# Kernel optimization log

Measured on AMD Instinct MI355X. Metric: run time of the kernel, lower is better.

## Reference

```python
import jax, jax.numpy as jnp
import numpy as np

N, E, K = 1048576, 64, 8        # tokens, experts, top-k
TEMP = 1.0                       # default temperature_scheduler returns 1.0
NEG = -1e16                      # masked-logit fill from the original code
EPS = 1e-8


def setup_inputs() -> dict:
    key = jax.random.key(0)
    k1, k2 = jax.random.split(key)
    inputs = jax.random.normal(k1, (N, E), dtype=jnp.float32)
    # Gumbel noise exactly as sample_gumbel(): -log(-log(U + 1e-8) + 1e-8)
    u = jax.random.uniform(k2, (N, E), dtype=jnp.float32)
    noise = -jnp.log(-jnp.log(u + EPS) + EPS)
    return {"inputs": inputs, "noise": noise}


def reference(inputs, noise):
    # Gumbel-perturbed softmax over experts (training path)
    probs = jax.nn.softmax((inputs + noise) / TEMP, axis=1)          # [N, E]
    # top-k expert selection on perturbed probs (indices only matter)
    _, top_k_idx = jax.lax.top_k(probs, K)                           # [N, K]
    # one-hot-sum mask built via scatter instead of materializing [N, K, E]
    rows = jnp.arange(inputs.shape[0])[:, None]                      # [N, 1]
    mask = jnp.zeros_like(inputs).at[rows, top_k_idx].set(1.0)       # [N, E]
    # keep ORIGINAL (un-noised) logits at selected experts, -1e16 elsewhere
    sparse_inputs = jnp.where(mask > 0.0, inputs, NEG)
    # renormalize over the selected experts
    return jax.nn.softmax(sparse_inputs, axis=1)
```

## Files before the change

### kernel.cpp

```cpp
#include <hip/hip_runtime.h>
#include <cstdint>

typedef float float4v __attribute__((ext_vector_type(4)));

__device__ __forceinline__ uint32_t mono32(float x) {
    int32_t b = __float_as_int(x);
    return (uint32_t)(b ^ ((b >> 31) | 0x80000000));
}

__global__ __launch_bounds__(256, 4)
void gumbel_topk_softmax_kernel(const float* __restrict__ gin,
                                const float* __restrict__ gnz,
                                float* __restrict__ gout) {
    const int t   = threadIdx.x;
    const int c   = t & 3;
    const size_t row = (size_t)blockIdx.x * 64 + (t >> 2);
    const size_t base = row * 64 + (size_t)c * 16;

    const float4v* a4 = (const float4v*)(gin + base);
    const float4v* b4 = (const float4v*)(gnz + base);

    float4v vin[4], vnz[4];
#pragma unroll
    for (int q = 0; q < 4; ++q) vin[q] = a4[q];
#pragma unroll
    for (int q = 0; q < 4; ++q) vnz[q] = b4[q];

    float keys[16];
    float heap[8];
#pragma unroll
    for (int u = 0; u < 8; ++u) heap[u] = -INFINITY;
#pragma unroll
    for (int q = 0; q < 4; ++q)
#pragma unroll
        for (int i = 0; i < 4; ++i) {
            float s = vin[q][i] + vnz[q][i];
            keys[q * 4 + i] = s;
#pragma unroll
            for (int u = 0; u < 8; ++u) {
                float h = heap[u];
                heap[u] = fmaxf(h, s);
                s       = fminf(h, s);
            }
        }

#define CEX(A, B) { float mx = fmaxf(heap[A], heap[B]);                       \
                    float mn = fminf(heap[A], heap[B]);                       \
                    heap[A] = mx; heap[B] = mn; }
#pragma unroll
    for (int m = 1; m <= 2; m <<= 1) {
        float part[8];
#pragma unroll
        for (int u = 0; u < 8; ++u) part[u] = __shfl_xor(heap[7 - u], m);
#pragma unroll
        for (int u = 0; u < 8; ++u) heap[u] = fmaxf(heap[u], part[u]);
        CEX(0, 4) CEX(1, 5) CEX(2, 6) CEX(3, 7)
        CEX(0, 2) CEX(1, 3) CEX(4, 6) CEX(5, 7)
        CEX(0, 1) CEX(2, 3) CEX(4, 5) CEX(6, 7)
    }
#undef CEX

    const float T = heap[7];
    uint32_t m16 = 0u;
    int cnt = 0;
#pragma unroll
    for (int j = 0; j < 16; ++j) {
        bool ge = keys[j] >= T;
        cnt += ge ? 1 : 0;
        m16 |= ge ? (1u << j) : 0u;
    }
    cnt += __shfl_xor(cnt, 1);
    cnt += __shfl_xor(cnt, 2);

    if (cnt != 8) {
        unsigned long long h8[8];
#pragma unroll
        for (int u = 0; u < 8; ++u) h8[u] = 0ull;
        const float* ar = gin + row * 64;
        const float* br = gnz + row * 64;
#pragma unroll
        for (int j = 0; j < 64; ++j) {
            float a = ar[j], b = br[j];
            float s  = a + b;
            float ap = s - b;
            float bp = s - ap;
            float res = (a - ap) + (b - bp);
            unsigned long long key = ((unsigned long long)mono32(s) << 32)
                                   | ((unsigned long long)(mono32(res) >> 6) << 6)
                                   | (unsigned long long)(63 - j);
#pragma unroll
            for (int u = 0; u < 8; ++u) {
                unsigned long long hq = h8[u];
                unsigned long long mx = key > hq ? key : hq;
                key   = key > hq ? hq : key;
                h8[u] = mx;
            }
        }
        unsigned long long mask64 = 0ull;
#pragma unroll
        for (int u = 0; u < 8; ++u) mask64 |= 1ull << (63 - (int)(h8[u] & 63ull));
        m16 = (uint32_t)((mask64 >> (c * 16)) & 0xFFFFull);
    }

    float4v ev[4];
    float ssum = 0.f;
#pragma unroll
    for (int q = 0; q < 4; ++q)
#pragma unroll
        for (int i = 0; i < 4; ++i) {
            float e = __expf(vin[q][i]) * (float)((m16 >> (q * 4 + i)) & 1u);
            ev[q][i] = e;
            ssum += e;
        }
    ssum += __shfl_xor(ssum, 1);
    ssum += __shfl_xor(ssum, 2);
    const float inv = 1.0f / ssum;

    float4v* o4 = (float4v*)(gout + base);
#pragma unroll
    for (int q = 0; q < 4; ++q) {
        float4v v;
#pragma unroll
        for (int i = 0; i < 4; ++i) v[i] = ev[q][i] * inv;
        o4[q] = v;
    }
}

extern "C" void kernel_launch(void* const* d_in, const int* in_sizes, int n_in,
                              void* d_out, int out_size, void* d_ws, size_t ws_size,
                              hipStream_t stream) {
    const float* gin = (const float*)d_in[0];
    const float* gnz = (const float*)d_in[1];
    float* gout = (float*)d_out;
    const int nrows = in_sizes[0] / 64;
    const int grid  = nrows / 64;
    gumbel_topk_softmax_kernel<<<grid, 256, 0, stream>>>(gin, gnz, gout);
}
```

Measured before the change: 160.9 us.

## Make blocks persistent over 8 row tiles with double-buffered register prefetch

Changes the launch to a fixed 2048-block grid in which each block walks 8 tiles of 64 rows, strided by the grid size. The next tile's input and noise are loaded into a second register set while the current tile is processed, to hide memory latency. Output stores become nontemporal. The grid is now hardcoded and assumes N = 2048*8*64 rows, and the extra register buffers may lower occupancy.

Result: slower. 395.1 us (+145.5%).

```diff
diff --git a/kernel.cpp b/kernel.cpp
--- a/kernel.cpp
+++ b/kernel.cpp
@@ -8,121 +8,141 @@
     return (uint32_t)(b ^ ((b >> 31) | 0x80000000));
 }
 
+#define GRID  2048
+#define TPB   8
+
 __global__ __launch_bounds__(256, 4)
 void gumbel_topk_softmax_kernel(const float* __restrict__ gin,
                                 const float* __restrict__ gnz,
                                 float* __restrict__ gout) {
-    const int t   = threadIdx.x;
-    const int c   = t & 3;
-    const size_t row = (size_t)blockIdx.x * 64 + (t >> 2);
-    const size_t base = row * 64 + (size_t)c * 16;
+    const int t = threadIdx.x;
+    const int c = t & 3;
+    const int rl = t >> 2;
 
-    const float4v* a4 = (const float4v*)(gin + base);
-    const float4v* b4 = (const float4v*)(gnz + base);
+    auto tbase = [&](int i) -> size_t {
+        return ((size_t)(blockIdx.x + (size_t)i * GRID) * 64 + rl) * 64
+             + (size_t)c * 16;
+    };
 
-    float4v vin[4], vnz[4];
+    auto LOAD = [&](size_t b, float4v (&A)[4], float4v (&N)[4]) {
+        const float4v* a4 = (const float4v*)(gin + b);
+        const float4v* n4 = (const float4v*)(gnz + b);
 #pragma unroll
-    for (int q = 0; q < 4; ++q) vin[q] = a4[q];
+        for (int q = 0; q < 4; ++q) A[q] = a4[q];
 #pragma unroll
-    for (int q = 0; q < 4; ++q) vnz[q] = b4[q];
+        for (int q = 0; q < 4; ++q) N[q] = n4[q];
+    };
 
-    float keys[16];
-    float heap[8];
+    auto BODY = [&](const float4v (&vin)[4], const float4v (&vnz)[4], size_t base) {
+        float keys[16];
+        float heap[8];
 #pragma unroll
-    for (int u = 0; u < 8; ++u) heap[u] = -INFINITY;
+        for (int u = 0; u < 8; ++u) heap[u] = -INFINITY;
 #pragma unroll
-    for (int q = 0; q < 4; ++q)
+        for (int q = 0; q < 4; ++q)
 #pragma unroll
-        for (int i = 0; i < 4; ++i) {
-            float s = vin[q][i] + vnz[q][i];
-            keys[q * 4 + i] = s;
+            for (int i = 0; i < 4; ++i) {
+                float s = vin[q][i] + vnz[q][i];
+                keys[q * 4 + i] = s;
 #pragma unroll
-            for (int u = 0; u < 8; ++u) {
-                float h = heap[u];
-                heap[u] = fmaxf(h, s);
-                s       = fminf(h, s);
+                for (int u = 0; u < 8; ++u) {
+                    float h = heap[u];
+                    heap[u] = fmaxf(h, s);
+                    s       = fminf(h, s);
+                }
             }
+
+#define CEX(A, B) { float mx = fmaxf(heap[A], heap[B]);                        \
+                    float mn = fminf(heap[A], heap[B]);                        \
+                    heap[A] = mx; heap[B] = mn; }
+#pragma unroll
+        for (int m = 1; m <= 2; m <<= 1) {
+            float part[8];
+#pragma unroll
+            for (int u = 0; u < 8; ++u) part[u] = __shfl_xor(heap[7 - u], m);
+#pragma unroll
+            for (int u = 0; u < 8; ++u) heap[u] = fmaxf(heap[u], part[u]);
+            CEX(0, 4) CEX(1, 5) CEX(2, 6) CEX(3, 7)
+            CEX(0, 2) CEX(1, 3) CEX(4, 6) CEX(5, 7)
+            CEX(0, 1) CEX(2, 3) CEX(4, 5) CEX(6, 7)
+        }
+#undef CEX
+
+        const float T = heap[7];
+        uint32_t m16 = 0u;
+        int cnt = 0;
+#pragma unroll
+        for (int j = 0; j < 16; ++j) {
+            bool ge = keys[j] >= T;
+            cnt += ge ? 1 : 0;
+            m16 |= ge ? (1u << j) : 0u;
+        }
+        cnt += __shfl_xor(cnt, 1);
+        cnt += __shfl_xor(cnt, 2);
+
+        if (cnt != 8) {
+            unsigned long long h8[8];
+#pragma unroll
+            for (int u = 0; u < 8; ++u) h8[u] = 0ull;
+            const float* ar = gin + (base - (size_t)c * 16);
+            const float* br = gnz + (base - (size_t)c * 16);
+#pragma unroll
+            for (int j = 0; j < 64; ++j) {
+                float a = ar[j], b = br[j];
+                float s  = a + b;
+                float ap = s - b;
+                float bp = s - ap;
+                float res = (a - ap) + (b - bp);
+                unsigned long long key = ((unsigned long long)mono32(s) << 32)
+                                       | ((unsigned long long)(mono32(res) >> 6) << 6)
+                                       | (unsigned long long)(63 - j);
+#pragma unroll
+                for (int u = 0; u < 8; ++u) {
+                    unsigned long long hq = h8[u];
+                    unsigned long long mx = key > hq ? key : hq;
+                    key   = key > hq ? hq : key;
+                    h8[u] = mx;
+                }
+            }
+            unsigned long long mask64 = 0ull;
+#pragma unroll
+            for (int u = 0; u < 8; ++u)
+                mask64 |= 1ull << (63 - (int)(h8[u] & 63ull));
+            m16 = (uint32_t)((mask64 >> (c * 16)) & 0xFFFFull);
         }
 
-#define CEX(A, B) { float mx = fmaxf(heap[A], heap[B]);                       \
-                    float mn = fminf(heap[A], heap[B]);                       \
-                    heap[A] = mx; heap[B] = mn; }
+        float4v ev[4];
+        float ssum = 0.f;
 #pragma unroll
-    for (int m = 1; m <= 2; m <<= 1) {
-        float part[8];
+        for (int q = 0; q < 4; ++q)
 #pragma unroll
-        for (int u = 0; u < 8; ++u) part[u] = __shfl_xor(heap[7 - u], m);
+            for (int i = 0; i < 4; ++i) {
+                float e = __expf(vin[q][i]) * (float)((m16 >> (q * 4 + i)) & 1u);
+                ev[q][i] = e;
+                ssum += e;
+            }
+        ssum += __shfl_xor(ssum, 1);
+        ssum += __shfl_xor(ssum, 2);
+        const float inv = 1.0f / ssum;
+
+        float4v* o4 = (float4v*)(gout + base);
 #pragma unroll
-        for (int u = 0; u < 8; ++u) heap[u] = fmaxf(heap[u], part[u]);
-        CEX(0, 4) CEX(1, 5) CEX(2, 6) CEX(3, 7)
-        CEX(0, 2) CEX(1, 3) CEX(4, 6) CEX(5, 7)
-        CEX(0, 1) CEX(2, 3) CEX(4, 5) CEX(6, 7)
-    }
-#undef CEX
+        for (int q = 0; q < 4; ++q) {
+            float4v v;
+#pragma unroll
+            for (int i = 0; i < 4; ++i) v[i] = ev[q][i] * inv;
+            __builtin_nontemporal_store(v, o4 + q);
+        }
+    };
 
-    const float T = heap[7];
-    uint32_t m16 = 0u;
-    int cnt = 0;
+    float4v A0[4], N0[4], A1[4], N1[4];
+    LOAD(tbase(0), A0, N0);
 #pragma unroll
-    for (int j = 0; j < 16; ++j) {
-        bool ge = keys[j] >= T;
-        cnt += ge ? 1 : 0;
-        m16 |= ge ? (1u << j) : 0u;
-    }
-    cnt += __shfl_xor(cnt, 1);
-    cnt += __shfl_xor(cnt, 2);
-
-    if (cnt != 8) {
-        unsigned long long h8[8];
-#pragma unroll
-        for (int u = 0; u < 8; ++u) h8[u] = 0ull;
-        const float* ar = gin + row * 64;
-        const float* br = gnz + row * 64;
-#pragma unroll
-        for (int j = 0; j < 64; ++j) {
-            float a = ar[j], b = br[j];
-            float s  = a + b;
-            float ap = s - b;
-            float bp = s - ap;
-            float res = (a - ap) + (b - bp);
-            unsigned long long key = ((unsigned long long)mono32(s) << 32)
-                                   | ((unsigned long long)(mono32(res) >> 6) << 6)
-                                   | (unsigned long long)(63 - j);
-#pragma unroll
-            for (int u = 0; u < 8; ++u) {
-                unsigned long long hq = h8[u];
-                unsigned long long mx = key > hq ? key : hq;
-                key   = key > hq ? hq : key;
-                h8[u] = mx;
-            }
-        }
-        unsigned long long mask64 = 0ull;
-#pragma unroll
-        for (int u = 0; u < 8; ++u) mask64 |= 1ull << (63 - (int)(h8[u] & 63ull));
-        m16 = (uint32_t)((mask64 >> (c * 16)) & 0xFFFFull);
-    }
-
-    float4v ev[4];
-    float ssum = 0.f;
-#pragma unroll
-    for (int q = 0; q < 4; ++q)
-#pragma unroll
-        for (int i = 0; i < 4; ++i) {
-            float e = __expf(vin[q][i]) * (float)((m16 >> (q * 4 + i)) & 1u);
-            ev[q][i] = e;
-            ssum += e;
-        }
-    ssum += __shfl_xor(ssum, 1);
-    ssum += __shfl_xor(ssum, 2);
-    const float inv = 1.0f / ssum;
-
-    float4v* o4 = (float4v*)(gout + base);
-#pragma unroll
-    for (int q = 0; q < 4; ++q) {
-        float4v v;
-#pragma unroll
-        for (int i = 0; i < 4; ++i) v[i] = ev[q][i] * inv;
-        o4[q] = v;
+    for (int p = 0; p < TPB; p += 2) {
+        if (p + 1 < TPB) LOAD(tbase(p + 1), A1, N1);
+        BODY(A0, N0, tbase(p));
+        if (p + 2 < TPB) LOAD(tbase(p + 2), A0, N0);
+        BODY(A1, N1, tbase(p + 1));
     }
 }
 
@@ -132,7 +152,5 @@
     const float* gin = (const float*)d_in[0];
     const float* gnz = (const float*)d_in[1];
     float* gout = (float*)d_out;
-    const int nrows = in_sizes[0] / 64;
-    const int grid  = nrows / 64;
-    gumbel_topk_softmax_kernel<<<grid, 256, 0, stream>>>(gin, gnz, gout);
+    gumbel_topk_softmax_kernel<<<GRID, 256, 0, stream>>>(gin, gnz, gout);
 }
```
